# Kernel tuning notes

Hardware: AMD Instinct MI355X
Metric: run time of the kernel (lower is better)

The kernel has to match this reference:

```python
import jax, jax.numpy as jnp
import numpy as np

H = 4096        # hidden_size
NH = 32         # num query heads
NG = 8          # num query groups (kv heads)
HD = H // NH    # head size = 128
B, S = 2, 2048


def gen_rope_cache(seq_length, n_elem, base=10000.0):
    theta = 1.0 / base ** (jnp.arange(0, n_elem, 2, dtype=jnp.float32) / n_elem)
    idx_theta = jnp.outer(jnp.arange(seq_length, dtype=jnp.float32), theta)
    return jnp.stack([jnp.cos(idx_theta), jnp.sin(idx_theta)], axis=-1)  # [S, n_elem//2, 2]


def apply_rope(x, cache):
    # x: [B, S, nh, hd], cache: [S, hd//2, 2]; rot_dim == hd (no pass-through)
    b, s, nh, hd = x.shape
    xr = x.reshape(b, s, nh, hd // 2, 2)
    c = cache[:s].reshape(1, s, 1, hd // 2, 2)
    out = jnp.stack([
        xr[..., 0] * c[..., 0] - xr[..., 1] * c[..., 1],
        xr[..., 1] * c[..., 0] + xr[..., 0] * c[..., 1],
    ], axis=-1)
    return out.reshape(b, s, nh, hd)


def setup_inputs() -> dict:
    key = jax.random.key(0)
    k1, k2, k3, k4 = jax.random.split(key, 4)
    x = jax.random.normal(k1, (B, S, H), dtype=jnp.float32)
    W_qkv = jax.random.normal(k2, (H, H + 2 * NG * HD), dtype=jnp.float32) * 0.02
    b_qkv = jax.random.normal(k3, (H + 2 * NG * HD,), dtype=jnp.float32) * 0.02
    W_dense = jax.random.normal(k4, (H, H), dtype=jnp.float32) * 0.02
    rope_cache = gen_rope_cache(S, HD)
    return {"x": x, "rope_cache": rope_cache, "W_qkv": W_qkv, "b_qkv": b_qkv, "W_dense": W_dense}


def reference(x, rope_cache, W_qkv, b_qkv, W_dense):
    b, s, h = x.shape
    qkv = jnp.einsum('bsh,ho->bso', x, W_qkv) + b_qkv
    q, k, v = jnp.split(qkv, [h, h + NG * HD], axis=-1)
    q = q.reshape(b, s, NH, HD)
    k = k.reshape(b, s, NG, HD)
    v = v.reshape(b, s, NG, HD)
    q = apply_rope(q, rope_cache)
    k = apply_rope(k, rope_cache)
    # GQA: group query heads [B, G, rep, S, D] against kv [B, G, S, D]
    rep = NH // NG
    qg = q.transpose(0, 2, 1, 3).reshape(b, NG, rep, s, HD)
    kg = k.transpose(0, 2, 1, 3)  # [B, G, S, D]
    vg = v.transpose(0, 2, 1, 3)
    scale = 1.0 / jnp.sqrt(jnp.float32(HD))
    scores = jnp.einsum('bgrqd,bgkd->bgrqk', qg, kg) * scale
    causal = jnp.tril(jnp.ones((s, s), dtype=bool))
    scores = jnp.where(causal, scores, jnp.float32(-1e30))
    attn = jax.nn.softmax(scores, axis=-1)
    out = jnp.einsum('bgrqk,bgkd->bgrqd', attn, vg)  # [B, G, rep, S, D]
    out = out.reshape(b, NH, s, HD).transpose(0, 2, 1, 3).reshape(b, s, h)
    return jnp.einsum('bsh,ho->bso', out, W_dense)
```

## Files before the change

### kernel.cpp

```cpp
#include <hip/hip_runtime.h>
#include <hip/hip_bf16.h>
#include <math.h>

#define BS   4096
#define HH   4096
#define NH   32
#define NG   8
#define HD   128
#define SEQ  2048
#define NQKV 6144

typedef float f32x4 __attribute__((ext_vector_type(4)));
typedef float f32x16 __attribute__((ext_vector_type(16)));
typedef short s16x8 __attribute__((ext_vector_type(8)));
typedef short s16x4 __attribute__((ext_vector_type(4)));
typedef unsigned int u32x4 __attribute__((ext_vector_type(4)));

__device__ __forceinline__ unsigned short f2bf(float f) {
  unsigned int u = __builtin_bit_cast(unsigned int, f);
  unsigned int r = (u + 0x7fffu + ((u >> 16) & 1u)) >> 16;
  return (unsigned short)r;
}
__device__ __forceinline__ float b2f(short h) {
  unsigned int u = ((unsigned int)(unsigned short)h) << 16;
  return __builtin_bit_cast(float, u);
}

__device__ __forceinline__ void gload16(const void* g, void* l) {
  __builtin_amdgcn_global_load_lds((__attribute__((address_space(1))) void*)(g),
                                   (__attribute__((address_space(3))) void*)(l), 16, 0, 0);
}

#define BARRIER __builtin_amdgcn_s_barrier()
#define PRIO1 __builtin_amdgcn_s_setprio(1)
#define PRIO0 __builtin_amdgcn_s_setprio(0)

__global__ void cast_f32_bf16(const float* __restrict__ in, short* __restrict__ out, long n4) {
  long i = (long)blockIdx.x * blockDim.x + threadIdx.x;
  long stride = (long)gridDim.x * blockDim.x;
  for (; i < n4; i += stride) {
    float4 v = *(const float4*)&in[i * 4];
    s16x4 o;
    o[0] = (short)f2bf(v.x); o[1] = (short)f2bf(v.y);
    o[2] = (short)f2bf(v.z); o[3] = (short)f2bf(v.w);
    *(s16x4*)&out[i * 4] = o;
  }
}

__global__ __launch_bounds__(256) void transpose_cast(const float* __restrict__ in,
                                                      short* __restrict__ out, int R, int C) {
  __shared__ float tile[32][33];
  int tx = threadIdx.x & 31, ty = threadIdx.x >> 5;
  long c0 = (long)blockIdx.x * 32, r0 = (long)blockIdx.y * 32;
#pragma unroll
  for (int j = 0; j < 32; j += 8)
    tile[ty + j][tx] = in[(r0 + ty + j) * C + c0 + tx];
  __syncthreads();
#pragma unroll
  for (int j = 0; j < 32; j += 8)
    out[(c0 + ty + j) * R + r0 + tx] = (short)f2bf(tile[tx][ty + j]);
}

#define LDA_FR(BASE, DB)                                                         \
  {                                                                              \
    _Pragma("unroll") for (int mf = 0; mf < 4; ++mf)                             \
      _Pragma("unroll") for (int ks = 0; ks < 2; ++ks)                           \
        af[mf][ks] = *(const s16x8*)&lds[(BASE) + (DB) * 8192 + aoff[mf][ks]];   \
  }
#define LDB_FR(BASE, DB)                                                         \
  {                                                                              \
    _Pragma("unroll") for (int nf = 0; nf < 2; ++nf)                             \
      _Pragma("unroll") for (int ks = 0; ks < 2; ++ks)                           \
        bf[nf][ks] = *(const s16x8*)&lds[(BASE) + (DB) * 8192 + boff[nf][ks]];   \
  }
#define MF_Q(MS, NS)                                                             \
  {                                                                              \
    _Pragma("unroll") for (int ks = 0; ks < 2; ++ks)                             \
      _Pragma("unroll") for (int mf = 0; mf < 4; ++mf)                           \
        _Pragma("unroll") for (int nf = 0; nf < 2; ++nf)                         \
          acc[(MS) * 4 + mf][(NS) * 2 + nf] = __builtin_amdgcn_mfma_f32_16x16x32_bf16( \
              af[mf][ks], bf[nf][ks], acc[(MS) * 4 + mf][(NS) * 2 + nf], 0, 0, 0);     \
  }
#define STG_AU0(DB, KB) { gload16(sA0 + (KB), &lds[0 + (DB) * 8192 + du0]);            \
                          gload16(sA1 + (KB), &lds[0 + (DB) * 8192 + du1]); }
#define STG_BU0(DB, KB) { gload16(sB0 + (KB), &lds[32768 + (DB) * 8192 + du0]);        \
                          gload16(sB1 + (KB), &lds[32768 + (DB) * 8192 + du1]); }
#define STG_AU1(DB, KB) { gload16(sA0 + 64 * (long)K + (KB), &lds[16384 + (DB) * 8192 + du0]); \
                          gload16(sA1 + 64 * (long)K + (KB), &lds[16384 + (DB) * 8192 + du1]); }
#define STG_BU1(DB, KB) { gload16(sB0 + 32 * (long)K + (KB), &lds[49152 + (DB) * 8192 + du0]); \
                          gload16(sB1 + 32 * (long)K + (KB), &lds[49152 + (DB) * 8192 + du1]); }

#define TILE256(DB, KBS)                                                         \
  LDA_FR(0, DB); LDB_FR(32768, DB);                                              \
  STG_AU0(DB ^ 1, KBS); STG_BU0(DB ^ 1, KBS);                                    \
  BARRIER;                                                                       \
  PRIO1; MF_Q(0, 0); PRIO0;                                                      \
  asm volatile("s_waitcnt vmcnt(6)" ::: "memory");                               \
  BARRIER;                                                                       \
  LDB_FR(49152, DB);                                                             \
  STG_BU1(DB ^ 1, KBS);                                                          \
  BARRIER;                                                                       \
  PRIO1; MF_Q(0, 1); PRIO0;                                                      \
  asm volatile("s_waitcnt vmcnt(6)" ::: "memory");                               \
  BARRIER;                                                                       \
  LDA_FR(16384, DB);                                                             \
  STG_AU1(DB ^ 1, KBS);                                                          \
  BARRIER;                                                                       \
  PRIO1; MF_Q(1, 1); PRIO0;                                                      \
  BARRIER;                                                                       \
  LDB_FR(32768, DB);                                                             \
  BARRIER;                                                                       \
  PRIO1; MF_Q(1, 0); PRIO0;                                                      \
  asm volatile("s_waitcnt vmcnt(4)" ::: "memory");                               \
  BARRIER;

template <int MODE>
__global__ __launch_bounds__(512, 1) void gemm256(const short* __restrict__ A,
                                                  const short* __restrict__ Bt,
                                                  const float* __restrict__ bias,
                                                  void* __restrict__ Cout,
                                                  const float* __restrict__ cache,
                                                  short* __restrict__ Qb,
                                                  int M, int N, int K) {
  extern __shared__ short lds[];
  const int t = threadIdx.x;
  const int lane = t & 63, w = t >> 6;
  const int g = lane >> 4, lr = lane & 15;
  const int wm = w >> 2, wn = w & 3;
  const long bm = (long)blockIdx.y * 256;
  const long bn = (long)blockIdx.x * 256;

  const short *sA0, *sA1, *sB0, *sB1;
  {
    int c0 = t, c1 = t + 512;
    int h0 = c0 >> 9, r0 = (c0 >> 3) & 63, tc0 = (c0 & 7) ^ (r0 & 7);
    int h1 = c1 >> 9, r1 = (c1 >> 3) & 63, tc1 = (c1 & 7) ^ (r1 & 7);
    sA0 = A + (bm + h0 * 128 + r0) * (long)K + tc0 * 8;
    sA1 = A + (bm + h1 * 128 + r1) * (long)K + tc1 * 8;
    int g0 = c0 >> 8, rb0 = (c0 >> 3) & 31, tb0 = (c0 & 7) ^ (rb0 & 7);
    int g1 = c1 >> 8, rb1 = (c1 >> 3) & 31, tb1 = (c1 & 7) ^ (rb1 & 7);
    sB0 = Bt + (bn + g0 * 64 + rb0) * (long)K + tb0 * 8;
    sB1 = Bt + (bn + g1 * 64 + rb1) * (long)K + tb1 * 8;
  }
  const int du0 = w * 512;
  const int du1 = w * 512 + 4096;

  int aoff[4][2], boff[2][2];
#pragma unroll
  for (int mf = 0; mf < 4; ++mf)
#pragma unroll
    for (int ks = 0; ks < 2; ++ks)
      aoff[mf][ks] = wm * 4096 + (mf * 16 + lr) * 64 + (((ks * 4 + g) ^ (lr & 7)) * 8);
#pragma unroll
  for (int nf = 0; nf < 2; ++nf)
#pragma unroll
    for (int ks = 0; ks < 2; ++ks)
      boff[nf][ks] = wn * 2048 + (nf * 16 + lr) * 64 + (((ks * 4 + g) ^ (lr & 7)) * 8);

  f32x4 acc[8][4] = {};
  s16x8 af[4][2], bf[2][2];

  STG_AU0(0, 0); STG_BU0(0, 0); STG_AU1(0, 0); STG_BU1(0, 0);
  asm volatile("s_waitcnt vmcnt(0)" ::: "memory");
  BARRIER;

  const int NT = K >> 6;
  for (int kt = 0; kt < NT; kt += 2) {
    const long kb1 = (long)(kt + 1) * 64;
    const long kb2 = (kt + 2 < NT) ? (long)(kt + 2) * 64 : 0l;
    TILE256(0, kb1);
    TILE256(1, kb2);
  }

  if (MODE == 0) {
#pragma unroll
    for (int am = 0; am < 8; ++am) {
      long row = bm + wm * 128 + am * 16 + g * 4;
#pragma unroll
      for (int an = 0; an < 4; ++an) {
        long col = bn + wn * 64 + an * 16 + lr;
#pragma unroll
        for (int r = 0; r < 4; ++r)
          ((float*)Cout)[(row + r) * N + col] = acc[am][an][r];
      }
    }
  } else {
    const float scq = 0.12751743f;
#pragma unroll
    for (int am = 0; am < 8; ++am) {
      int row0 = (int)bm + wm * 128 + am * 16 + g * 4;
      int s0 = row0 & (SEQ - 1);
      int bb = row0 >> 11;
#pragma unroll
      for (int an = 0; an < 4; ++an) {
        int col = (int)bn + wn * 64 + an * 16 + lr;
        float bv = bias[col];
        int h = col >> 7, d = col & 127;
        const int odd = lr & 1;
#pragma unroll
        for (int r = 0; r < 4; ++r) {
          float v = acc[am][an][r] + bv;
          float p = __shfl_xor(v, 1);
          float2 cs = *(const float2*)&cache[((long)(s0 + r) * 64 + (d >> 1)) * 2];
          float o = odd ? (v * cs.x + p * cs.y) : (v * cs.x - p * cs.y);
          Qb[((long)(bb * NH + h) * SEQ + s0 + r) * HD + d] = (short)f2bf(o * scq);
        }
      }
    }
  }
}

#define KV_LDA(MSB, DB, KS)                                                      \
  { _Pragma("unroll") for (int mf = 0; mf < 4; ++mf)                             \
      af[mf] = *(const s16x8*)&lds[(MSB) + (DB) * 8192 + aoff[mf][KS]]; }
#define KV_LDB(DB, KS)                                                           \
  { _Pragma("unroll") for (int nf = 0; nf < 2; ++nf)                             \
      bfk[nf] = *(const s16x8*)&lds[32768 + (DB) * 8192 + boff[nf][KS]]; }
#define KV_MF(MS)                                                                \
  { _Pragma("unroll") for (int mf = 0; mf < 4; ++mf)                             \
      _Pragma("unroll") for (int nf = 0; nf < 2; ++nf)                           \
        acc[(MS) * 4 + mf][nf] = __builtin_amdgcn_mfma_f32_16x16x32_bf16(        \
            af[mf], bfk[nf], acc[(MS) * 4 + mf][nf], 0, 0, 0); }
#define KV_SA0(DB, KB) { gload16(sA0 + (KB), &lds[(DB) * 8192 + du0]);                 \
                         gload16(sA1 + (KB), &lds[(DB) * 8192 + du1]); }
#define KV_SA1(DB, KB) { gload16(sA0 + 64 * (long)HH + (KB), &lds[16384 + (DB) * 8192 + du0]); \
                         gload16(sA1 + 64 * (long)HH + (KB), &lds[16384 + (DB) * 8192 + du1]); }
#define KV_SB(DB, KB)  { gload16(sB0 + (KB), &lds[32768 + (DB) * 8192 + du0]);         \
                         gload16(sB1 + (KB), &lds[32768 + (DB) * 8192 + du1]); }

#define KVTILE(DB, KBS)                                                          \
  KV_LDA(0, DB, 0); KV_LDB(DB, 0);                                               \
  KV_SA0(DB ^ 1, KBS);                                                           \
  BARRIER;                                                                       \
  PRIO1; KV_MF(0); PRIO0;                                                        \
  asm volatile("s_waitcnt vmcnt(2)" ::: "memory");                               \
  BARRIER;                                                                       \
  KV_LDA(16384, DB, 0);                                                          \
  KV_SB(DB ^ 1, KBS);                                                            \
  BARRIER;                                                                       \
  PRIO1; KV_MF(1); PRIO0;                                                        \
  BARRIER;                                                                       \
  KV_LDA(16384, DB, 1); KV_LDB(DB, 1);                                           \
  KV_SA1(DB ^ 1, KBS);                                                           \
  BARRIER;                                                                       \
  PRIO1; KV_MF(1); PRIO0;                                                        \
  BARRIER;                                                                       \
  KV_LDA(0, DB, 1);                                                              \
  BARRIER;                                                                       \
  PRIO1; KV_MF(0); PRIO0;                                                        \
  asm volatile("s_waitcnt vmcnt(2)" ::: "memory");                               \
  BARRIER;

__global__ __launch_bounds__(512, 1) void gemm_kv(const short* __restrict__ A,
                                                  const short* __restrict__ Bt,
                                                  const float* __restrict__ bias,
                                                  const float* __restrict__ cache,
                                                  short* __restrict__ Kb,
                                                  short* __restrict__ Vtb) {
  extern __shared__ short lds[];
  const int t = threadIdx.x;
  const int lane = t & 63, w = t >> 6;
  const int g = lane >> 4, lr = lane & 15;
  const int wm = w >> 2, wn = w & 3;
  const long bm = (long)blockIdx.y * 256;
  const int bnl = blockIdx.x * 128;

  const short *sA0, *sA1, *sB0, *sB1;
  {
    int c0 = t, c1 = t + 512;
    int h0 = c0 >> 9, r0 = (c0 >> 3) & 63, tc0 = (c0 & 7) ^ (r0 & 7);
    int h1 = c1 >> 9, r1 = (c1 >> 3) & 63, tc1 = (c1 & 7) ^ (r1 & 7);
    sA0 = A + (bm + h0 * 128 + r0) * (long)HH + tc0 * 8;
    sA1 = A + (bm + h1 * 128 + r1) * (long)HH + tc1 * 8;
    int rb0 = c0 >> 3, tb0 = (c0 & 7) ^ (rb0 & 7);
    int rb1 = c1 >> 3, tb1 = (c1 & 7) ^ (rb1 & 7);
    sB0 = Bt + ((long)bnl + rb0) * HH + tb0 * 8;
    sB1 = Bt + ((long)bnl + rb1) * HH + tb1 * 8;
  }
  const int du0 = w * 512;
  const int du1 = w * 512 + 4096;

  int aoff[4][2], boff[2][2];
#pragma unroll
  for (int mf = 0; mf < 4; ++mf)
#pragma unroll
    for (int ks = 0; ks < 2; ++ks)
      aoff[mf][ks] = wm * 4096 + (mf * 16 + lr) * 64 + (((ks * 4 + g) ^ (lr & 7)) * 8);
#pragma unroll
  for (int nf = 0; nf < 2; ++nf)
#pragma unroll
    for (int ks = 0; ks < 2; ++ks)
      boff[nf][ks] = wn * 2048 + (nf * 16 + lr) * 64 + (((ks * 4 + g) ^ (lr & 7)) * 8);

  f32x4 acc[8][2] = {};
  s16x8 af[4], bfk[2];

  KV_SA0(0, 0); KV_SB(0, 0); KV_SA1(0, 0);
  asm volatile("s_waitcnt vmcnt(0)" ::: "memory");
  BARRIER;

  for (int kt = 0; kt < 64; kt += 2) {
    const long kb1 = (long)(kt + 1) * 64;
    const long kb2 = (kt + 2 < 64) ? (long)(kt + 2) * 64 : 0l;
    KVTILE(0, kb1);
    KVTILE(1, kb2);
  }

#pragma unroll
  for (int am = 0; am < 8; ++am) {
    int row0 = (int)bm + wm * 128 + am * 16 + g * 4;
    int s0 = row0 & (SEQ - 1);
    int bb = row0 >> 11;
#pragma unroll
    for (int an = 0; an < 2; ++an) {
      int cl = bnl + wn * 32 + an * 16 + lr;
      float bv = bias[4096 + cl];
      if (cl < 1024) {
        int gi = cl >> 7, d = cl & 127;
        const int odd = lr & 1;
#pragma unroll
        for (int r = 0; r < 4; ++r) {
          float v = acc[am][an][r] + bv;
          float p = __shfl_xor(v, 1);
          float2 cs = *(const float2*)&cache[((long)(s0 + r) * 64 + (d >> 1)) * 2];
          float o = odd ? (v * cs.x + p * cs.y) : (v * cs.x - p * cs.y);
          Kb[((long)(bb * NG + gi) * SEQ + s0 + r) * HD + d] = (short)f2bf(o);
        }
      } else {
        int cv = cl - 1024;
        int gi = cv >> 7, d = cv & 127;
        s16x4 o;
#pragma unroll
        for (int r = 0; r < 4; ++r) o[r] = (short)f2bf(acc[am][an][r] + bv);
        *(s16x4*)&Vtb[((long)(bb * NG + gi) * HD + d) * SEQ + s0] = o;
      }
    }
  }
}

__global__ __launch_bounds__(512, 1) void attn(const short* __restrict__ Qb,
                                               const short* __restrict__ Kb,
                                               const short* __restrict__ Vtb,
                                               short* __restrict__ Ob) {
  extern __shared__ short alds[];
  const int t = threadIdx.x, lane = t & 63, w = t >> 6;
  const int l31 = lane & 31, hi = lane >> 5;
  const int bid = (int)blockIdx.x;
  const int q0 = (bid >> 1) & 3;
  const int qt = ((bid ^ (bid >> 8)) & 1) ? 7 - q0 : q0;
  const int head = (bid >> 3) & 63;
  const int b = head >> 5, h = head & 31;
  const int qb = qt * 256;
  const short* Qhead = Qb + (long)(b * NH + h) * SEQ * HD;
  const short* Khead = Kb + (long)(b * NG + (h >> 2)) * SEQ * HD;
  const short* Vthead = Vtb + (long)(b * NG + (h >> 2)) * SEQ * HD;
  const int qw0 = qb + w * 32;
  const int qrow = qw0 + l31;
  float* facs = (float*)&alds[32768] + w * 32;

  s16x8 qf[8];
#pragma unroll
  for (int ds = 0; ds < 8; ++ds)
    qf[ds] = *(const s16x8*)&Qhead[(long)qrow * HD + ds * 16 + hi * 8];

  const short *kp0, *kp1, *vp0, *vp1;
  {
    int c0 = t, c1 = t + 512;
    int kr0 = c0 >> 4, kc0 = (c0 & 15) ^ (kr0 & 15);
    int kr1 = c1 >> 4, kc1 = (c1 & 15) ^ (kr1 & 15);
    kp0 = Khead + (long)kr0 * HD + kc0 * 8;
    kp1 = Khead + (long)kr1 * HD + kc1 * 8;
    int vr0 = c0 >> 3, vc0 = (c0 & 7) ^ (vr0 & 7);
    int vr1 = c1 >> 3, vc1 = (c1 & 7) ^ (vr1 & 7);
    vp0 = Vthead + (long)vr0 * SEQ + vc0 * 8;
    vp1 = Vthead + (long)vr1 * SEQ + vc1 * 8;
  }
  const int d0 = w * 512, d1 = w * 512 + 4096;

  f32x16 ao[4] = {};
  float mrun = -1.0e30f, lrun = 0.0f;
  const int nkt = 4 * qt + 4;

  gload16(kp0, &alds[d0]); gload16(kp1, &alds[d1]);
  gload16(vp0, &alds[16384 + d0]); gload16(vp1, &alds[16384 + d1]);
  kp0 += 64 * HD; kp1 += 64 * HD; vp0 += 64; vp1 += 64;
  asm volatile("s_waitcnt vmcnt(0)" ::: "memory");
  BARRIER;

  for (int kt = 0; kt < nkt; ++kt) {
    const int buf = kt & 1, nb = buf ^ 1;
    const int kb = kt * 64;
    const int bK = buf * 8192, bV = 16384 + buf * 8192;
    if (kt + 1 < nkt) {
      gload16(kp0, &alds[nb * 8192 + d0]); gload16(kp1, &alds[nb * 8192 + d1]);
      gload16(vp0, &alds[16384 + nb * 8192 + d0]); gload16(vp1, &alds[16384 + nb * 8192 + d1]);
      kp0 += 64 * HD; kp1 += 64 * HD; vp0 += 64; vp1 += 64;
    }
    if (kb <= qw0 + 31) {
      f32x16 st0 = {}, st1 = {};
      PRIO1;
#pragma unroll
      for (int ds = 0; ds < 8; ++ds) {
        const int c = ds * 2 + hi;
        const int r0 = l31, r1 = 32 + l31;
        s16x8 kf0 = *(const s16x8*)&alds[bK + r0 * 128 + ((c ^ (r0 & 15)) * 8)];
        s16x8 kf1 = *(const s16x8*)&alds[bK + r1 * 128 + ((c ^ (r1 & 15)) * 8)];
        st0 = __builtin_amdgcn_mfma_f32_32x32x16_bf16(kf0, qf[ds], st0, 0, 0, 0);
        st1 = __builtin_amdgcn_mfma_f32_32x32x16_bf16(kf1, qf[ds], st1, 0, 0, 0);
      }
      PRIO0;

      float p[32];
      if (kb + 63 > qrow || kb + 63 > qw0) {
#pragma unroll
        for (int r = 0; r < 16; ++r) {
          int kg = kb + (r & 3) + 8 * (r >> 2) + 4 * hi;
          p[r] = (kg > qrow) ? -1.0e30f : st0[r];
          p[16 + r] = (kg + 32 > qrow) ? -1.0e30f : st1[r];
        }
      } else {
#pragma unroll
        for (int r = 0; r < 16; ++r) { p[r] = st0[r]; p[16 + r] = st1[r]; }
      }
      float tmax = -1.0e30f;
#pragma unroll
      for (int i = 0; i < 32; ++i) tmax = fmaxf(tmax, p[i]);
      tmax = fmaxf(tmax, __shfl_xor(tmax, 32));
      if (!__all(tmax <= mrun + 8.0f)) {
        float mnew = fmaxf(mrun, tmax);
        float fac = exp2f(mrun - mnew);
        facs[l31] = fac;
        mrun = mnew; lrun *= fac;
        f32x4 f0 = *(f32x4*)&facs[0 + 4 * hi];
        f32x4 f1 = *(f32x4*)&facs[8 + 4 * hi];
        f32x4 f2 = *(f32x4*)&facs[16 + 4 * hi];
        f32x4 f3 = *(f32x4*)&facs[24 + 4 * hi];
#pragma unroll
        for (int j = 0; j < 4; ++j)
#pragma unroll
          for (int dt = 0; dt < 4; ++dt) {
            ao[dt][j] *= f0[j]; ao[dt][4 + j] *= f1[j];
            ao[dt][8 + j] *= f2[j]; ao[dt][12 + j] *= f3[j];
          }
      }
      float tsum = 0.0f;
#pragma unroll
      for (int i = 0; i < 32; ++i) { p[i] = exp2f(p[i] - mrun); tsum += p[i]; }
      lrun += tsum + __shfl_xor(tsum, 32);

      s16x8 pa[4];
#pragma unroll
      for (int ks = 0; ks < 4; ++ks) {
        unsigned w0, w1, w2, w3;
        asm("v_cvt_pk_bf16_f32 %0, %1, %2" : "=v"(w0) : "v"(p[ks * 8 + 0]), "v"(p[ks * 8 + 1]));
        asm("v_cvt_pk_bf16_f32 %0, %1, %2" : "=v"(w1) : "v"(p[ks * 8 + 2]), "v"(p[ks * 8 + 3]));
        asm("v_cvt_pk_bf16_f32 %0, %1, %2" : "=v"(w2) : "v"(p[ks * 8 + 4]), "v"(p[ks * 8 + 5]));
        asm("v_cvt_pk_bf16_f32 %0, %1, %2" : "=v"(w3) : "v"(p[ks * 8 + 6]), "v"(p[ks * 8 + 7]));
        unsigned sw0 = (unsigned)__shfl_xor((int)w0, 32);
        unsigned sw1 = (unsigned)__shfl_xor((int)w1, 32);
        unsigned sw2 = (unsigned)__shfl_xor((int)w2, 32);
        unsigned sw3 = (unsigned)__shfl_xor((int)w3, 32);
        u32x4 pw;
        pw[0] = hi ? sw2 : w0;
        pw[1] = hi ? sw3 : w1;
        pw[2] = hi ? w2 : sw0;
        pw[3] = hi ? w3 : sw1;
        pa[ks] = __builtin_bit_cast(s16x8, pw);
      }

      PRIO1;
#pragma unroll
      for (int ks = 0; ks < 4; ++ks)
#pragma unroll
        for (int dt = 0; dt < 4; ++dt) {
          int dd = dt * 32 + l31;
          int slot = (ks * 2 + hi) ^ (dd & 7);
          s16x8 vf = *(const s16x8*)&alds[bV + dd * 64 + slot * 8];
          ao[dt] = __builtin_amdgcn_mfma_f32_32x32x16_bf16(pa[ks], vf, ao[dt], 0, 0, 0);
        }
      PRIO0;
    }
    asm volatile("s_waitcnt vmcnt(0)" ::: "memory");
    BARRIER;
  }

  facs[l31] = 1.0f / lrun;
  float invr[16];
  {
    f32x4 i0 = *(f32x4*)&facs[0 + 4 * hi];
    f32x4 i1 = *(f32x4*)&facs[8 + 4 * hi];
    f32x4 i2 = *(f32x4*)&facs[16 + 4 * hi];
    f32x4 i3 = *(f32x4*)&facs[24 + 4 * hi];
#pragma unroll
    for (int j = 0; j < 4; ++j) {
      invr[j] = i0[j]; invr[4 + j] = i1[j]; invr[8 + j] = i2[j]; invr[12 + j] = i3[j];
    }
  }
#pragma unroll
  for (int dt = 0; dt < 4; ++dt)
#pragma unroll
    for (int r = 0; r < 16; ++r) {
      int grow = qw0 + (r & 3) + 8 * (r >> 2) + 4 * hi;
      Ob[((long)b * SEQ + grow) * HH + h * HD + dt * 32 + l31] = (short)f2bf(ao[dt][r] * invr[r]);
    }
}

extern "C" void kernel_launch(void* const* d_in, const int* in_sizes, int n_in,
                              void* d_out, int out_size, void* d_ws, size_t ws_size,
                              hipStream_t stream) {
  const float* x     = (const float*)d_in[0];
  const float* cache = (const float*)d_in[1];
  const float* Wqkv  = (const float*)d_in[2];
  const float* bqkv  = (const float*)d_in[3];
  const float* Wd    = (const float*)d_in[4];

  char* ws = (char*)d_ws;
  short* xb   = (short*)(ws);
  short* wqt  = (short*)(ws + 33554432ll);
  short* wdt  = (short*)(ws + 83886080ll);
  short* Qb   = (short*)(ws + 167772160ll);
  short* Kb   = (short*)(ws + 201326592ll);
  short* Vtb  = (short*)(ws + 218103808ll);
  short* Ob   = (short*)(ws + 226492416ll);

  cast_f32_bf16<<<2048, 256, 0, stream>>>(x, xb, (long)BS * HH / 4);
  transpose_cast<<<dim3(NQKV / 32, HH / 32), 256, 0, stream>>>(Wqkv, wqt, HH, NQKV);
  transpose_cast<<<dim3(HH / 32, HH / 32), 256, 0, stream>>>(Wd, wdt, HH, HH);
  gemm256<2><<<dim3(16, 16), 512, 131072, stream>>>(
      xb, wqt, bqkv, nullptr, cache, Qb, BS, HH, HH);
  gemm_kv<<<dim3(16, 16), 512, 98304, stream>>>(
      xb, wqt + 4096ll * HH, bqkv, cache, Kb, Vtb);
  attn<<<512, 512, 66560, stream>>>(Qb, Kb, Vtb, Ob);
  gemm256<0><<<dim3(16, 16), 512, 131072, stream>>>(
      Ob, wdt, nullptr, d_out, nullptr, nullptr, BS, HH, HH);
}
```

Before: 485.0 us.

## Vectorize transpose stores, tree-reduce softmax max/sum, drop MFMA priority hints

The transpose-cast kernel now writes four bf16 values per thread as one 8-byte store instead of four scattered 2-byte stores. In the attention loop, the serial max and sum reductions over 32 scores become pairwise tree reductions, which shortens the dependency chain. The s_setprio raise/lower hints around the QK and PV MFMA blocks are removed. The tree sum changes float summation order slightly, and dropping the priority hints may change how waves interleave.

```diff
diff --git a/kernel.cpp b/kernel.cpp
--- a/kernel.cpp
+++ b/kernel.cpp
@@ -56,9 +56,14 @@
   for (int j = 0; j < 32; j += 8)
     tile[ty + j][tx] = in[(r0 + ty + j) * C + c0 + tx];
   __syncthreads();
-#pragma unroll
-  for (int j = 0; j < 32; j += 8)
-    out[(c0 + ty + j) * R + r0 + tx] = (short)f2bf(tile[tx][ty + j]);
+  int q = threadIdx.x & 7;
+  int jj = threadIdx.x >> 3;
+  s16x4 o;
+  o[0] = (short)f2bf(tile[4 * q + 0][jj]);
+  o[1] = (short)f2bf(tile[4 * q + 1][jj]);
+  o[2] = (short)f2bf(tile[4 * q + 2][jj]);
+  o[3] = (short)f2bf(tile[4 * q + 3][jj]);
+  *(s16x4*)&out[(c0 + jj) * R + r0 + 4 * q] = o;
 }
 
 #define LDA_FR(BASE, DB)                                                         \
@@ -398,7 +403,6 @@
     }
     if (kb <= qw0 + 31) {
       f32x16 st0 = {}, st1 = {};
-      PRIO1;
 #pragma unroll
       for (int ds = 0; ds < 8; ++ds) {
         const int c = ds * 2 + hi;
@@ -408,7 +412,6 @@
         st0 = __builtin_amdgcn_mfma_f32_32x32x16_bf16(kf0, qf[ds], st0, 0, 0, 0);
         st1 = __builtin_amdgcn_mfma_f32_32x32x16_bf16(kf1, qf[ds], st1, 0, 0, 0);
       }
-      PRIO0;
 
       float p[32];
       if (kb + 63 > qrow || kb + 63 > qw0) {
@@ -422,9 +425,15 @@
 #pragma unroll
         for (int r = 0; r < 16; ++r) { p[r] = st0[r]; p[16 + r] = st1[r]; }
       }
-      float tmax = -1.0e30f;
-#pragma unroll
-      for (int i = 0; i < 32; ++i) tmax = fmaxf(tmax, p[i]);
+      float tt[16];
+#pragma unroll
+      for (int i = 0; i < 16; ++i) tt[i] = fmaxf(p[i], p[i + 16]);
+#pragma unroll
+      for (int s = 8; s >= 1; s >>= 1)
+#pragma unroll
+        for (int i = 0; i < 8; ++i)
+          if (i < s) tt[i] = fmaxf(tt[i], tt[i + s]);
+      float tmax = tt[0];
       tmax = fmaxf(tmax, __shfl_xor(tmax, 32));
       if (!__all(tmax <= mrun + 8.0f)) {
         float mnew = fmaxf(mrun, tmax);
@@ -443,9 +452,17 @@
             ao[dt][8 + j] *= f2[j]; ao[dt][12 + j] *= f3[j];
           }
       }
-      float tsum = 0.0f;
-#pragma unroll
-      for (int i = 0; i < 32; ++i) { p[i] = exp2f(p[i] - mrun); tsum += p[i]; }
+#pragma unroll
+      for (int i = 0; i < 32; ++i) p[i] = exp2f(p[i] - mrun);
+      float ss[16];
+#pragma unroll
+      for (int i = 0; i < 16; ++i) ss[i] = p[i] + p[i + 16];
+#pragma unroll
+      for (int s = 8; s >= 1; s >>= 1)
+#pragma unroll
+        for (int i = 0; i < 8; ++i)
+          if (i < s) ss[i] = ss[i] + ss[i + s];
+      float tsum = ss[0];
       lrun += tsum + __shfl_xor(tsum, 32);
 
       s16x8 pa[4];
@@ -468,7 +485,6 @@
         pa[ks] = __builtin_bit_cast(s16x8, pw);
       }
 
-      PRIO1;
 #pragma unroll
       for (int ks = 0; ks < 4; ++ks)
 #pragma unroll
@@ -478,7 +494,6 @@
           s16x8 vf = *(const s16x8*)&alds[bV + dd * 64 + slot * 8];
           ao[dt] = __builtin_amdgcn_mfma_f32_32x32x16_bf16(pa[ks], vf, ao[dt], 0, 0, 0);
         }
-      PRIO0;
     }
     asm volatile("s_waitcnt vmcnt(0)" ::: "memory");
     BARRIER;
```

Result: no change. 487.4 us (+0.5%).
